# Kernel tuning notes

Hardware: AMD Instinct MI355X
Metric: run time of the kernel (lower is better)

Reference implementation:

```python
import jax, jax.numpy as jnp
import numpy as np

C = 128          # num_channel
NEI = 9          # patch_size / neighbor
R = NEI // 2     # displacement radius (4)
B, H, W = 4, 200, 200


def conv2d(x, w, b, pad):
    # x: [N,C,H,W], w: [O,I,kh,kw]
    y = jax.lax.conv_general_dilated(
        x, w, window_strides=(1, 1), padding=[(pad, pad), (pad, pad)],
        dimension_numbers=('NCHW', 'OIHW', 'NCHW'))
    return y + b[None, :, None, None]


def setup_inputs() -> dict:
    key = jax.random.key(0)
    ks = jax.random.split(key, 16)
    s = 0.02
    return {
        'feature_select': jax.random.normal(ks[0], (B, C, H, W), jnp.float32),
        'feature_current': jax.random.normal(ks[1], (B, C, H, W), jnp.float32),
        # embedding convs
        'ec1_w': jax.random.normal(ks[2], (64, C, 1, 1), jnp.float32) * s,
        'ec1_b': jnp.zeros((64,), jnp.float32),
        'ec2_w': jax.random.normal(ks[3], (64, 64, 3, 3), jnp.float32) * s,
        'ec2_b': jnp.zeros((64,), jnp.float32),
        # aggregation convs
        'ag1_w': jax.random.normal(ks[4], (64, C, 1, 1), jnp.float32) * s,
        'ag1_b': jnp.zeros((64,), jnp.float32),
        'ag2_w': jax.random.normal(ks[5], (32, 64, 3, 3), jnp.float32) * s,
        'ag2_b': jnp.zeros((32,), jnp.float32),
        'ag3_w': jax.random.normal(ks[6], (1, 32, 1, 1), jnp.float32) * s,
        'ag3_b': jnp.zeros((1,), jnp.float32),
    }


def reference(feature_select, feature_current, ec1_w, ec1_b, ec2_w, ec2_b,
              ag1_w, ag1_b, ag2_w, ag2_b, ag3_w, ag3_b):
    b, c, h, w = feature_select.shape
    # --- shared embedding network ---
    cat = jnp.concatenate([feature_select, feature_current], axis=0)
    e = jax.nn.relu(conv2d(cat, ec1_w, ec1_b, 0))
    e = jax.nn.relu(conv2d(e, ec2_w, ec2_b, 1))
    e_sel, e_cur = e[:b], e[b:]   # (torch code names these current/select, order follows concat)
    # --- correlation: 9x9 patch, kernel_size=1, zero-padded displaced neighbors ---
    ep = jnp.pad(e_cur, ((0, 0), (0, 0), (R, R), (R, R)))
    corr = []
    for di in range(-R, R + 1):
        for dj in range(-R, R + 1):
            nb = ep[:, :, R + di:R + di + h, R + dj:R + dj + w]
            corr.append(jnp.sum(e_sel * nb, axis=1))  # [b,h,w]
    weights = jax.nn.softmax(jnp.stack(corr, axis=1), axis=1)  # [b,81,h,w]
    # --- neighbor-weighted feature alignment ---
    sp = jnp.pad(feature_select, ((0, 0), (0, 0), (R, R), (R, R)))
    align = jnp.zeros_like(feature_select)
    k = 0
    for di in range(-R, R + 1):
        for dj in range(-R, R + 1):
            align = align + weights[:, k:k + 1] * sp[:, :, R + di:R + di + h, R + dj:R + dj + w]
            k += 1
    # --- aggregation: adaptive 2-way blend ---
    fc = jnp.concatenate([align, feature_current], axis=0)
    a = jax.nn.relu(conv2d(fc, ag1_w, ag1_b, 0))
    a = jax.nn.relu(conv2d(a, ag2_w, ag2_b, 1))
    a = jax.nn.relu(conv2d(a, ag3_w, ag3_b, 0))  # [2b,1,h,w]
    w2 = jax.nn.softmax(jnp.concatenate([a[:b], a[b:]], axis=1), axis=1)
    return w2[:, 0:1] * align + w2[:, 1:2] * feature_current
```

## Files before the change

### kernel.cpp

```cpp
#include <hip/hip_runtime.h>

namespace {
constexpr int H = 200, W = 200, HW = H * W;
constexpr int Bz = 4;
constexpr int PW = 208, PH = 202, PPLANE = PW * PH;
constexpr int EPW = 208, EPH = 208, EPL = EPW * EPH;
constexpr int WST = 88;
}

typedef __attribute__((ext_vector_type(8))) short bf16x8;
typedef __attribute__((ext_vector_type(4))) float f32x4;

__device__ inline ushort f2bf(float f) {
  unsigned u = __float_as_uint(f);
  u += 0x7fffu + ((u >> 16) & 1u);
  return (ushort)(u >> 16);
}

__global__ __launch_bounds__(256) void zero_k(uint4* __restrict__ p, int n) {
  int i = blockIdx.x * 256 + threadIdx.x;
  if (i < n) p[i] = uint4{0u, 0u, 0u, 0u};
}

__global__ __launch_bounds__(256) void wxform_k(const float* __restrict__ w,
                                                ushort* __restrict__ wb, int cout) {
  int i = blockIdx.x * 256 + threadIdx.x;
  int tot = cout * 64 * 9;
  if (i >= tot) return;
  int co = i / (64 * 9);
  int r = i % (64 * 9);
  int ci = r / 9, tap = r % 9;
  wb[(tap * cout + co) * 64 + ci] = f2bf(w[i]);
}

template <int CIN>
__global__ __launch_bounds__(256) void conv1x1_nhwc_k(
    const float* __restrict__ srcA, const float* __restrict__ srcB,
    const float* __restrict__ w, const float* __restrict__ bias,
    ushort* __restrict__ out) {
  __shared__ float wt[CIN * 64];
  for (int i = threadIdx.x; i < CIN * 64; i += 256) {
    int ci = i >> 6, co = i & 63;
    wt[i] = w[co * CIN + ci];
  }
  __syncthreads();
  int p = blockIdx.x * 256 + threadIdx.x;
  int bb = p / HW, pix = p % HW;
  const float* src =
      (bb < Bz ? srcA + (size_t)bb * CIN * HW : srcB + (size_t)(bb - Bz) * CIN * HW) + pix;
  float acc[64];
#pragma unroll
  for (int co = 0; co < 64; co++) acc[co] = bias[co];
  for (int ci = 0; ci < CIN; ci++) {
    float x = src[(size_t)ci * HW];
    const float4* w4 = (const float4*)&wt[ci * 64];
#pragma unroll
    for (int q = 0; q < 16; q++) {
      float4 wv = w4[q];
      acc[4 * q + 0] += x * wv.x;
      acc[4 * q + 1] += x * wv.y;
      acc[4 * q + 2] += x * wv.z;
      acc[4 * q + 3] += x * wv.w;
    }
  }
  int y = pix / W, x = pix % W;
  ushort* o = out + ((size_t)bb * PPLANE + (size_t)(y + 1) * PW + (x + 1)) * 64;
  uint4* o4 = (uint4*)o;
#pragma unroll
  for (int g = 0; g < 8; g++) {
    unsigned u0 = (unsigned)f2bf(fmaxf(acc[8 * g + 0], 0.f)) |
                  ((unsigned)f2bf(fmaxf(acc[8 * g + 1], 0.f)) << 16);
    unsigned u1 = (unsigned)f2bf(fmaxf(acc[8 * g + 2], 0.f)) |
                  ((unsigned)f2bf(fmaxf(acc[8 * g + 3], 0.f)) << 16);
    unsigned u2 = (unsigned)f2bf(fmaxf(acc[8 * g + 4], 0.f)) |
                  ((unsigned)f2bf(fmaxf(acc[8 * g + 5], 0.f)) << 16);
    unsigned u3 = (unsigned)f2bf(fmaxf(acc[8 * g + 6], 0.f)) |
                  ((unsigned)f2bf(fmaxf(acc[8 * g + 7], 0.f)) << 16);
    o4[g] = uint4{u0, u1, u2, u3};
  }
}

template <int COUT, bool NHWC>
__global__ __launch_bounds__(256) void conv3x3_mfma_k(
    const ushort* __restrict__ in, const ushort* __restrict__ wb,
    const float* __restrict__ bias, float* __restrict__ outf,
    ushort* __restrict__ outh) {
  constexpr int NF = COUT / 16;
  __shared__ ushort As[272 * 72];
  __shared__ ushort Bs[3 * COUT * 64];
  const int tile = blockIdx.x, img = blockIdx.y;
  const int pp0 = PW + tile * 256;
  const int tid = threadIdx.x, wave = tid >> 6, lane = tid & 63;
  const int lm = lane & 15, lq = lane >> 4;
  const ushort* inb = in + (size_t)img * PPLANE * 64;

  f32x4 acc[4][NF];
#pragma unroll
  for (int mf = 0; mf < 4; mf++)
#pragma unroll
    for (int nf = 0; nf < NF; nf++) acc[mf][nf] = f32x4{0.f, 0.f, 0.f, 0.f};

  for (int dy = 0; dy < 3; dy++) {
    __syncthreads();
    long abase = ((long)pp0 + (long)(dy - 1) * PW - 8) * 64;
    for (int i = tid; i < 272 * 8; i += 256) {
      int m = i >> 3, kseg = i & 7;
      uint4 v = *(const uint4*)(inb + abase + (long)m * 64 + kseg * 8);
      *(uint4*)&As[m * 72 + kseg * 8] = v;
    }
    for (int i = tid; i < 3 * COUT * 8; i += 256) {
      int dx = i / (COUT * 8);
      int r = i % (COUT * 8);
      int co = r >> 3, kseg = r & 7;
      uint4 v = *(const uint4*)(wb + (((size_t)(dy * 3 + dx) * COUT + co) << 6) + kseg * 8);
      *(uint4*)&Bs[(dx * COUT + co) * 64 + ((kseg ^ (co & 7)) * 8)] = v;
    }
    __syncthreads();
#pragma unroll
    for (int dx = 0; dx < 3; dx++) {
#pragma unroll
      for (int kc = 0; kc < 2; kc++) {
        bf16x8 bfr[NF];
#pragma unroll
        for (int nf = 0; nf < NF; nf++) {
          int n = nf * 16 + lm;
          int kb = kc * 4 + lq;
          bfr[nf] = *(const bf16x8*)&Bs[(dx * COUT + n) * 64 + ((kb ^ (n & 7)) * 8)];
        }
#pragma unroll
        for (int mf = 0; mf < 4; mf++) {
          int mo = (wave * 4 + mf) * 16 + lm;
          bf16x8 afr = *(const bf16x8*)&As[(mo + dx + 7) * 72 + kc * 32 + lq * 8];
#pragma unroll
          for (int nf = 0; nf < NF; nf++)
            acc[mf][nf] = __builtin_amdgcn_mfma_f32_16x16x32_bf16(afr, bfr[nf],
                                                                  acc[mf][nf], 0, 0, 0);
        }
      }
    }
  }
  float bv[NF];
#pragma unroll
  for (int nf = 0; nf < NF; nf++) bv[nf] = bias[nf * 16 + lm];
#pragma unroll
  for (int mf = 0; mf < 4; mf++) {
#pragma unroll
    for (int nf = 0; nf < NF; nf++) {
      int co = nf * 16 + lm;
#pragma unroll
      for (int r = 0; r < 4; r++) {
        int mo = pp0 + (wave * 4 + mf) * 16 + lq * 4 + r;
        int py = mo / PW, px = mo % PW;
        if (py >= 1 && py <= H && px >= 1 && px <= W) {
          float v = fmaxf(acc[mf][nf][r] + bv[nf], 0.f);
          if (NHWC) {
            ushort* eo = outh + (size_t)img * EPL * 64;
            eo[(((size_t)(py + 3)) * EPW + (px + 3)) * 64 + co] = f2bf(v);
          } else {
            outf[((size_t)img * COUT + co) * HW + (py - 1) * W + (px - 1)] = v;
          }
        }
      }
    }
  }
}

__global__ __launch_bounds__(128) void corr_mfma_k(
    const ushort* __restrict__ e, ushort* __restrict__ wgt) {
  __shared__ float S[2 * 16 * 91];
  const int wave = threadIdx.x >> 6, lane = threadIdx.x & 63;
  const int x0 = blockIdx.x * 16;
  const int y = blockIdx.y * 2 + wave;
  const int b = blockIdx.z;
  const int nl = lane & 15, kq = lane >> 4;
  const ushort* es = e + (size_t)b * EPL * 64;
  const ushort* ec = e + (size_t)(b + 4) * EPL * 64;
  size_t abase = ((size_t)(y + 4) * EPW + (size_t)(4 + x0 + nl)) * 64 + kq * 8;
  bf16x8 afr0 = *(const bf16x8*)(es + abase);
  bf16x8 afr1 = *(const bf16x8*)(es + abase + 32);
  float* Sw = &S[wave * 16 * 91];
  for (int di = 0; di < 9; di++) {
    const ushort* erow = ec + ((size_t)(y + di) * EPW + x0) * 64;
#pragma unroll
    for (int nh = 0; nh < 2; nh++) {
      f32x4 g = f32x4{0.f, 0.f, 0.f, 0.f};
      const ushort* bp = erow + (size_t)(nh * 16 + nl) * 64 + kq * 8;
      bf16x8 b0 = *(const bf16x8*)(bp);
      bf16x8 b1 = *(const bf16x8*)(bp + 32);
      g = __builtin_amdgcn_mfma_f32_16x16x32_bf16(afr0, b0, g, 0, 0, 0);
      g = __builtin_amdgcn_mfma_f32_16x16x32_bf16(afr1, b1, g, 0, 0, 0);
      int q = nh * 16 + nl;
#pragma unroll
      for (int r = 0; r < 4; r++) {
        int m = kq * 4 + r;
        int s = q - m;
        if (s >= 0 && s <= 8) Sw[m * 91 + di * 9 + s] = g[r];
      }
    }
  }
  int px = lane >> 2, lg = lane & 3;
  float* Sp = &Sw[px * 91];
  float mx = -1e30f;
  for (int k = lg; k < 81; k += 4) mx = fmaxf(mx, Sp[k]);
  mx = fmaxf(mx, __shfl_xor(mx, 1));
  mx = fmaxf(mx, __shfl_xor(mx, 2));
  float sum = 0.f;
  for (int k = lg; k < 81; k += 4) {
    float t = expf(Sp[k] - mx);
    Sp[k] = t;
    sum += t;
  }
  sum += __shfl_xor(sum, 1);
  sum += __shfl_xor(sum, 2);
  float rinv = 1.f / sum;
  if (x0 + px < W) {
    ushort* wp = wgt + ((size_t)b * 40000 + (size_t)y * W + x0 + px) * WST;
    for (int k = lg; k < 81; k += 4) wp[k] = f2bf(Sp[k] * rinv);
  }
}

__global__ __launch_bounds__(256) void align_mfma_k(
    const ushort* __restrict__ wgt, const float* __restrict__ fs,
    float* __restrict__ out) {
  __shared__ ushort F[32 * 392];
  __shared__ ushort WT[128 * WST];
  const int x0 = blockIdx.x * 16, y0 = blockIdx.y * 8;
  const int b = blockIdx.z & 3, cs = blockIdx.z >> 2;
  const int c0 = cs * 32;
  const int tid = threadIdx.x;
  {
    const ushort* wb = wgt + (size_t)b * 40000 * WST;
    for (int i = tid; i < 1408; i += 256) {
      int row = i / 176, rem = i % 176;
      size_t src = ((size_t)(y0 + row) * W + x0) * WST + (size_t)rem * 8;
      *(uint4*)&WT[(size_t)row * 16 * WST + rem * 8] = *(const uint4*)(wb + src);
    }
  }
  const float* fb = fs + ((size_t)b * 128 + c0) * HW;
  for (int i = tid; i < 32 * 392; i += 256) {
    int c = i / 392, rem = i % 392;
    int row = rem / 24, pos = rem % 24;
    int gy = y0 + row - 4, gx = x0 + pos - 4;
    float v = (rem < 384 && gy >= 0 && gy < H && gx >= 0 && gx < W)
                  ? fb[(size_t)c * HW + gy * W + gx] : 0.f;
    F[c * 392 + rem] = f2bf(v);
  }
  __syncthreads();
  const int wave = tid >> 6, lane = tid & 63;
  const int nl = lane & 15, kq = lane >> 4;
  f32x4 acc[2][2];
#pragma unroll
  for (int s = 0; s < 2; s++)
#pragma unroll
    for (int cg = 0; cg < 2; cg++) acc[s][cg] = f32x4{0.f, 0.f, 0.f, 0.f};

#pragma unroll
  for (int s = 0; s < 2; s++) {
    int r = wave * 2 + s;
    const ushort* wrow = &WT[(size_t)(r * 16 + nl) * WST];
    for (int di = 0; di < 9; di++) {
      union { bf16x8 v; ushort u[8]; } A;
#pragma unroll
      for (int j = 0; j < 8; j++) {
        int t = kq * 8 + j - nl;
        int tc = t < 0 ? 0 : (t > 8 ? 8 : t);
        ushort wv = wrow[di * 9 + tc];
        A.u[j] = (t == tc) ? wv : (ushort)0;
      }
#pragma unroll
      for (int cg = 0; cg < 2; cg++) {
        bf16x8 bfr = *(const bf16x8*)&F[(size_t)(cg * 16 + nl) * 392 +
                                        (r + di) * 24 + kq * 8];
        acc[s][cg] =
            __builtin_amdgcn_mfma_f32_16x16x32_bf16(A.v, bfr, acc[s][cg], 0, 0, 0);
      }
    }
  }
  int mg = lane >> 4;
  int x4 = x0 + mg * 4;
  if (x4 + 3 < W) {
#pragma unroll
    for (int s = 0; s < 2; s++) {
      int yy = y0 + wave * 2 + s;
#pragma unroll
      for (int cg = 0; cg < 2; cg++) {
        int cgl = c0 + cg * 16 + nl;
        float4 st = float4{acc[s][cg][0], acc[s][cg][1], acc[s][cg][2], acc[s][cg][3]};
        *(float4*)&out[((size_t)b * 128 + cgl) * HW + (size_t)yy * W + x4] = st;
      }
    }
  }
}

__global__ __launch_bounds__(256) void final_k(
    const float* __restrict__ a2, const float* __restrict__ w3,
    const float* __restrict__ b3, const float* __restrict__ alignb,
    const float* __restrict__ fcur, float* __restrict__ out) {
  int p = blockIdx.x * 256 + threadIdx.x;
  int bb = p / HW, pix = p % HW;
  const float* aS = a2 + (size_t)bb * 32 * HW + pix;
  const float* aC = a2 + (size_t)(bb + Bz) * 32 * HW + pix;
  float s0 = b3[0], s1 = b3[0];
#pragma unroll
  for (int c = 0; c < 32; c++) {
    float wv = w3[c];
    s0 += wv * aS[(size_t)c * HW];
    s1 += wv * aC[(size_t)c * HW];
  }
  s0 = fmaxf(s0, 0.f);
  s1 = fmaxf(s1, 0.f);
  float m = fmaxf(s0, s1);
  float e0 = expf(s0 - m), e1 = expf(s1 - m);
  float inv = 1.f / (e0 + e1);
  float p0 = e0 * inv, p1 = e1 * inv;
  const float* al = alignb + (size_t)bb * 128 * HW + pix;
  const float* fc = fcur + (size_t)bb * 128 * HW + pix;
  float* o = out + (size_t)bb * 128 * HW + pix;
#pragma unroll 4
  for (int c = 0; c < 128; c++)
    o[(size_t)c * HW] = p0 * al[(size_t)c * HW] + p1 * fc[(size_t)c * HW];
}

extern "C" void kernel_launch(void* const* d_in, const int* in_sizes, int n_in,
                              void* d_out, int out_size, void* d_ws, size_t ws_size,
                              hipStream_t stream) {
  const float* fsel = (const float*)d_in[0];
  const float* fcur = (const float*)d_in[1];
  const float* ec1_w = (const float*)d_in[2];
  const float* ec1_b = (const float*)d_in[3];
  const float* ec2_w = (const float*)d_in[4];
  const float* ec2_b = (const float*)d_in[5];
  const float* ag1_w = (const float*)d_in[6];
  const float* ag1_b = (const float*)d_in[7];
  const float* ag2_w = (const float*)d_in[8];
  const float* ag2_b = (const float*)d_in[9];
  const float* ag3_w = (const float*)d_in[10];
  const float* ag3_b = (const float*)d_in[11];

  char* ws = (char*)d_ws;
  size_t off = 4096;
  ushort* padbuf = (ushort*)(ws + off);
  size_t padbuf_bytes = (size_t)8 * PPLANE * 64 * 2;
  off += padbuf_bytes;
  ushort* epad = (ushort*)(ws + off);
  size_t epad_bytes = (size_t)8 * EPL * 64 * 2;
  off += epad_bytes + 4096;
  ushort* wgtb = (ushort*)(ws + off);
  off += (size_t)4 * 40000 * WST * 2 + 4096;
  float* alignb = (float*)(ws + off);
  off += (size_t)4 * 128 * HW * 4;
  ushort* wb1 = (ushort*)(ws + off);
  off += 9 * 64 * 64 * 2;
  ushort* wb2 = (ushort*)(ws + off);
  off += 9 * 32 * 64 * 2;
  float* a2 = (float*)epad;
  float* outp = (float*)d_out;

  dim3 blk(256);
  const int MTILES = (200 * PW + 255) / 256;

  wxform_k<<<(9 * 64 * 64 + 255) / 256, blk, 0, stream>>>(ec2_w, wb1, 64);
  wxform_k<<<(9 * 32 * 64 + 255) / 256, blk, 0, stream>>>(ag2_w, wb2, 32);
  {
    int nz = (int)((padbuf_bytes + epad_bytes) / 16);
    zero_k<<<(nz + 255) / 256, blk, 0, stream>>>((uint4*)padbuf, nz);
  }
  conv1x1_nhwc_k<128><<<1250, blk, 0, stream>>>(fsel, fcur, ec1_w, ec1_b, padbuf);
  conv3x3_mfma_k<64, true><<<dim3(MTILES, 8), blk, 0, stream>>>(
      padbuf, wb1, ec2_b, nullptr, epad);
  corr_mfma_k<<<dim3(13, 100, 4), dim3(128), 0, stream>>>(epad, wgtb);
  align_mfma_k<<<dim3(13, 25, 16), blk, 0, stream>>>(wgtb, fsel, alignb);
  conv1x1_nhwc_k<128><<<1250, blk, 0, stream>>>(alignb, fcur, ag1_w, ag1_b, padbuf);
  conv3x3_mfma_k<32, false><<<dim3(MTILES, 8), blk, 0, stream>>>(
      padbuf, wb2, ag2_b, a2, nullptr);
  final_k<<<625, blk, 0, stream>>>(a2, ag3_w, ag3_b, alignb, fcur, outp);
}
```

Before: 902.0 us.

## Replace MFMA align kernel with VALU kernel using planar softmax weights

The correlation kernel now writes the softmax weights in a planar layout (81 planes per batch) instead of a per-pixel strided layout. The alignment kernel drops the banded-matrix MFMA formulation, which wasted most MMA lanes on zero padding. It becomes a VALU kernel where each block covers a 16x8 tile for all 128 channels in four chunks of 32, loading the weights once and keeping feature_select in fp32 in LDS. Blocks are also remapped across the XCDs for locality. This cuts redundant weight loads and the bf16 rounding of the features, at the cost of more scalar FMA work and larger LDS usage.

New measurement: 1.082 ms. 1.2x slower.

```diff
diff --git a/kernel.cpp b/kernel.cpp
--- a/kernel.cpp
+++ b/kernel.cpp
@@ -5,7 +5,6 @@
 constexpr int Bz = 4;
 constexpr int PW = 208, PH = 202, PPLANE = PW * PH;
 constexpr int EPW = 208, EPH = 208, EPL = EPW * EPH;
-constexpr int WST = 88;
 }
 
 typedef __attribute__((ext_vector_type(8))) short bf16x8;
@@ -214,79 +213,92 @@
   sum += __shfl_xor(sum, 2);
   float rinv = 1.f / sum;
   if (x0 + px < W) {
-    ushort* wp = wgt + ((size_t)b * 40000 + (size_t)y * W + x0 + px) * WST;
-    for (int k = lg; k < 81; k += 4) wp[k] = f2bf(Sp[k] * rinv);
-  }
-}
-
-__global__ __launch_bounds__(256) void align_mfma_k(
+    ushort* wp = wgt + (size_t)b * 81 * HW + (size_t)y * W + x0 + px;
+    for (int k = lg; k < 81; k += 4) wp[(size_t)k * HW] = f2bf(Sp[k] * rinv);
+  }
+}
+
+__global__ __launch_bounds__(256, 2) void align_valu_k(
     const ushort* __restrict__ wgt, const float* __restrict__ fs,
     float* __restrict__ out) {
-  __shared__ ushort F[32 * 392];
-  __shared__ ushort WT[128 * WST];
-  const int x0 = blockIdx.x * 16, y0 = blockIdx.y * 8;
-  const int b = blockIdx.z & 3, cs = blockIdx.z >> 2;
-  const int c0 = cs * 32;
+  __shared__ ushort Ws[81 * 128];
+  __shared__ float Fs[32 * 448];
   const int tid = threadIdx.x;
+  int orig = blockIdx.x + 25 * (blockIdx.y + 13 * blockIdx.z);
+  int xcd = orig & 7, idx = orig >> 3;
+  int wgid = (xcd < 4 ? xcd * 163 : 652 + (xcd - 4) * 162) + idx;
+  int by = wgid % 25;
+  int t2 = wgid / 25;
+  int bx = t2 % 13;
+  int b = t2 / 13;
+  const int x0 = bx * 16, y0 = by * 8;
+
   {
-    const ushort* wb = wgt + (size_t)b * 40000 * WST;
-    for (int i = tid; i < 1408; i += 256) {
-      int row = i / 176, rem = i % 176;
-      size_t src = ((size_t)(y0 + row) * W + x0) * WST + (size_t)rem * 8;
-      *(uint4*)&WT[(size_t)row * 16 * WST + rem * 8] = *(const uint4*)(wb + src);
-    }
-  }
-  const float* fb = fs + ((size_t)b * 128 + c0) * HW;
-  for (int i = tid; i < 32 * 392; i += 256) {
-    int c = i / 392, rem = i % 392;
-    int row = rem / 24, pos = rem % 24;
-    int gy = y0 + row - 4, gx = x0 + pos - 4;
-    float v = (rem < 384 && gy >= 0 && gy < H && gx >= 0 && gx < W)
-                  ? fb[(size_t)c * HW + gy * W + gx] : 0.f;
-    F[c * 392 + rem] = f2bf(v);
-  }
-  __syncthreads();
-  const int wave = tid >> 6, lane = tid & 63;
-  const int nl = lane & 15, kq = lane >> 4;
-  f32x4 acc[2][2];
-#pragma unroll
-  for (int s = 0; s < 2; s++)
-#pragma unroll
-    for (int cg = 0; cg < 2; cg++) acc[s][cg] = f32x4{0.f, 0.f, 0.f, 0.f};
-
-#pragma unroll
-  for (int s = 0; s < 2; s++) {
-    int r = wave * 2 + s;
-    const ushort* wrow = &WT[(size_t)(r * 16 + nl) * WST];
-    for (int di = 0; di < 9; di++) {
-      union { bf16x8 v; ushort u[8]; } A;
-#pragma unroll
-      for (int j = 0; j < 8; j++) {
-        int t = kq * 8 + j - nl;
-        int tc = t < 0 ? 0 : (t > 8 ? 8 : t);
-        ushort wv = wrow[di * 9 + tc];
-        A.u[j] = (t == tc) ? wv : (ushort)0;
-      }
-#pragma unroll
-      for (int cg = 0; cg < 2; cg++) {
-        bf16x8 bfr = *(const bf16x8*)&F[(size_t)(cg * 16 + nl) * 392 +
-                                        (r + di) * 24 + kq * 8];
-        acc[s][cg] =
-            __builtin_amdgcn_mfma_f32_16x16x32_bf16(A.v, bfr, acc[s][cg], 0, 0, 0);
-      }
-    }
-  }
-  int mg = lane >> 4;
-  int x4 = x0 + mg * 4;
-  if (x4 + 3 < W) {
-#pragma unroll
-    for (int s = 0; s < 2; s++) {
-      int yy = y0 + wave * 2 + s;
-#pragma unroll
-      for (int cg = 0; cg < 2; cg++) {
-        int cgl = c0 + cg * 16 + nl;
-        float4 st = float4{acc[s][cg][0], acc[s][cg][1], acc[s][cg][2], acc[s][cg][3]};
-        *(float4*)&out[((size_t)b * 128 + cgl) * HW + (size_t)yy * W + x4] = st;
+    const ushort* wb = wgt + (size_t)b * 81 * HW;
+    for (int i = tid; i < 81 * 128; i += 256) {
+      int k = i >> 7, px = i & 127;
+      int gy = y0 + (px >> 4);
+      int gx = x0 + (px & 15);
+      if (gx > W - 1) gx = W - 1;
+      Ws[i] = wb[(size_t)k * HW + gy * W + gx];
+    }
+  }
+  const int xq = tid & 3, yy = (tid >> 2) & 7, cl = tid >> 5;
+  const int pxw = yy * 16 + xq * 4;
+  const int xb = x0 + xq * 4;
+  for (int r = 0; r < 4; ++r) {
+    if (r) __syncthreads();
+    {
+      const float* fb = fs + ((size_t)b * 128 + r * 32) * HW;
+      for (int i = tid; i < 32 * 384; i += 256) {
+        int cc = i / 384, rem = i % 384;
+        int row = rem / 24, col = rem % 24;
+        int gy = y0 - 4 + row, gx = x0 - 4 + col;
+        float v = 0.f;
+        if (gy >= 0 && gy < H && gx >= 0 && gx < W)
+          v = fb[(size_t)cc * HW + gy * W + gx];
+        Fs[cc * 448 + row * 28 + col] = v;
+      }
+    }
+    __syncthreads();
+    float acc[4][4];
+#pragma unroll
+    for (int j = 0; j < 4; j++)
+#pragma unroll
+      for (int p = 0; p < 4; p++) acc[j][p] = 0.f;
+    for (int di = 0; di < 9; ++di) {
+      float fr[4][12];
+#pragma unroll
+      for (int j = 0; j < 4; ++j) {
+        const float4* fp =
+            (const float4*)&Fs[(cl * 4 + j) * 448 + (yy + di) * 28 + xq * 4];
+        float4 f0 = fp[0], f1 = fp[1], f2 = fp[2];
+        fr[j][0] = f0.x; fr[j][1] = f0.y; fr[j][2] = f0.z; fr[j][3] = f0.w;
+        fr[j][4] = f1.x; fr[j][5] = f1.y; fr[j][6] = f1.z; fr[j][7] = f1.w;
+        fr[j][8] = f2.x; fr[j][9] = f2.y; fr[j][10] = f2.z; fr[j][11] = f2.w;
+      }
+#pragma unroll
+      for (int dj = 0; dj < 9; ++dj) {
+        uint2 wv = *(const uint2*)&Ws[(di * 9 + dj) * 128 + pxw];
+        float w0 = __uint_as_float(wv.x << 16);
+        float w1 = __uint_as_float(wv.x & 0xffff0000u);
+        float w2 = __uint_as_float(wv.y << 16);
+        float w3 = __uint_as_float(wv.y & 0xffff0000u);
+#pragma unroll
+        for (int j = 0; j < 4; ++j) {
+          acc[j][0] += w0 * fr[j][dj + 0];
+          acc[j][1] += w1 * fr[j][dj + 1];
+          acc[j][2] += w2 * fr[j][dj + 2];
+          acc[j][3] += w3 * fr[j][dj + 3];
+        }
+      }
+    }
+    if (xb < W) {
+#pragma unroll
+      for (int j = 0; j < 4; ++j) {
+        int c = r * 32 + cl * 4 + j;
+        *(float4*)&out[((size_t)b * 128 + c) * HW + (size_t)(y0 + yy) * W + xb] =
+            float4{acc[j][0], acc[j][1], acc[j][2], acc[j][3]};
       }
     }
   }
@@ -346,7 +358,7 @@
   size_t epad_bytes = (size_t)8 * EPL * 64 * 2;
   off += epad_bytes + 4096;
   ushort* wgtb = (ushort*)(ws + off);
-  off += (size_t)4 * 40000 * WST * 2 + 4096;
+  off += (size_t)4 * 81 * HW * 2 + 4096;
   float* alignb = (float*)(ws + off);
   off += (size_t)4 * 128 * HW * 4;
   ushort* wb1 = (ushort*)(ws + off);
@@ -369,7 +381,7 @@
   conv3x3_mfma_k<64, true><<<dim3(MTILES, 8), blk, 0, stream>>>(
       padbuf, wb1, ec2_b, nullptr, epad);
   corr_mfma_k<<<dim3(13, 100, 4), dim3(128), 0, stream>>>(epad, wgtb);
-  align_mfma_k<<<dim3(13, 25, 16), blk, 0, stream>>>(wgtb, fsel, alignb);
+  align_valu_k<<<dim3(25, 13, 4), blk, 0, stream>>>(wgtb, fsel, alignb);
   conv1x1_nhwc_k<128><<<1250, blk, 0, stream>>>(alignb, fcur, ag1_w, ag1_b, padbuf);
   conv3x3_mfma_k<32, false><<<dim3(MTILES, 8), blk, 0, stream>>>(
       padbuf, wb2, ag2_b, a2, nullptr);
```

## Store softmax weights planar and rebuild align kernel with banded-weight LDS staging

Applied to the files above, without the earlier changes.

The correlation kernel now writes softmax weights in a planar [b][81][HW] layout instead of a per-pixel strided layout. The align kernel is rewritten to use 16x16 pixel tiles over 16 channels per block. It builds a banded weight matrix in LDS for each row displacement and prefetches the next displacement's weights into registers. The grid is a flat 1D launch ordered so that the batch/half index varies fastest, and occupancy is hinted at 3 blocks. This drops the per-lane select/clamp construction of A fragments and shrinks the weight buffer, at the cost of two barriers per displacement, strided per-plane weight reads, and more redundant feature halo loads for smaller channel groups.

Result: faster. 874.5 us (-3.1%).

```diff
diff --git a/kernel.cpp b/kernel.cpp
--- a/kernel.cpp
+++ b/kernel.cpp
@@ -5,7 +5,6 @@
 constexpr int Bz = 4;
 constexpr int PW = 208, PH = 202, PPLANE = PW * PH;
 constexpr int EPW = 208, EPH = 208, EPL = EPW * EPH;
-constexpr int WST = 88;
 }
 
 typedef __attribute__((ext_vector_type(8))) short bf16x8;
@@ -214,79 +213,92 @@
   sum += __shfl_xor(sum, 2);
   float rinv = 1.f / sum;
   if (x0 + px < W) {
-    ushort* wp = wgt + ((size_t)b * 40000 + (size_t)y * W + x0 + px) * WST;
-    for (int k = lg; k < 81; k += 4) wp[k] = f2bf(Sp[k] * rinv);
-  }
-}
-
-__global__ __launch_bounds__(256) void align_mfma_k(
+    ushort* wp = wgt + (size_t)b * 81 * HW + (size_t)y * W + x0 + px;
+    for (int k = lg; k < 81; k += 4) wp[(size_t)k * HW] = f2bf(Sp[k] * rinv);
+  }
+}
+
+__global__ __launch_bounds__(256, 3) void align_mfma2_k(
     const ushort* __restrict__ wgt, const float* __restrict__ fs,
     float* __restrict__ out) {
-  __shared__ ushort F[32 * 392];
-  __shared__ ushort WT[128 * WST];
-  const int x0 = blockIdx.x * 16, y0 = blockIdx.y * 8;
-  const int b = blockIdx.z & 3, cs = blockIdx.z >> 2;
-  const int c0 = cs * 32;
+  __shared__ alignas(16) ushort As2[16 * 16 * 40];
+  __shared__ alignas(16) ushort Fs2[24 * 16 * 40];
   const int tid = threadIdx.x;
+  int bid = blockIdx.x;
+  int p = bid & 7;
+  int rank = bid >> 3;
+  const int b = p >> 1, h = p & 1;
+  const int cgi = rank & 3;
+  int tile = rank >> 2;
+  const int ty = tile / 13, tx = tile % 13;
+  const int x0 = tx * 16, y0 = ty * 16;
+  const int c0 = (h * 4 + cgi) * 16;
+
+  for (int i = tid; i < 1280; i += 256) *(uint4*)&As2[i * 8] = uint4{0u, 0u, 0u, 0u};
+
+  const int srow = tid >> 4, sm = tid & 15;
+  const bool sval = (y0 + srow < H) && (x0 + sm < W);
+  const ushort* wrow =
+      wgt + (size_t)b * 81 * HW + (size_t)(y0 + srow) * W + (x0 + sm);
+  ushort wv[9];
+  if (sval) {
+#pragma unroll
+    for (int dj = 0; dj < 9; dj++) wv[dj] = wrow[(size_t)dj * HW];
+  }
+
   {
-    const ushort* wb = wgt + (size_t)b * 40000 * WST;
-    for (int i = tid; i < 1408; i += 256) {
-      int row = i / 176, rem = i % 176;
-      size_t src = ((size_t)(y0 + row) * W + x0) * WST + (size_t)rem * 8;
-      *(uint4*)&WT[(size_t)row * 16 * WST + rem * 8] = *(const uint4*)(wb + src);
-    }
-  }
-  const float* fb = fs + ((size_t)b * 128 + c0) * HW;
-  for (int i = tid; i < 32 * 392; i += 256) {
-    int c = i / 392, rem = i % 392;
-    int row = rem / 24, pos = rem % 24;
-    int gy = y0 + row - 4, gx = x0 + pos - 4;
-    float v = (rem < 384 && gy >= 0 && gy < H && gx >= 0 && gx < W)
-                  ? fb[(size_t)c * HW + gy * W + gx] : 0.f;
-    F[c * 392 + rem] = f2bf(v);
+    const float* fb = fs + ((size_t)b * 128 + c0) * HW;
+    for (int i = tid; i < 24 * 16 * 32; i += 256) {
+      int k = i & 31;
+      int c = (i >> 5) & 15;
+      int rf = i >> 9;
+      int gy = y0 - 4 + rf, gx = x0 - 4 + k;
+      float v = 0.f;
+      if (k < 24 && gy >= 0 && gy < H && gx >= 0 && gx < W)
+        v = fb[(size_t)c * HW + (size_t)gy * W + gx];
+      Fs2[(rf * 16 + c) * 40 + k] = f2bf(v);
+    }
   }
   __syncthreads();
-  const int wave = tid >> 6, lane = tid & 63;
+
+  const int lane = tid & 63, wave = tid >> 6;
   const int nl = lane & 15, kq = lane >> 4;
-  f32x4 acc[2][2];
-#pragma unroll
-  for (int s = 0; s < 2; s++)
-#pragma unroll
-    for (int cg = 0; cg < 2; cg++) acc[s][cg] = f32x4{0.f, 0.f, 0.f, 0.f};
-
-#pragma unroll
-  for (int s = 0; s < 2; s++) {
-    int r = wave * 2 + s;
-    const ushort* wrow = &WT[(size_t)(r * 16 + nl) * WST];
-    for (int di = 0; di < 9; di++) {
-      union { bf16x8 v; ushort u[8]; } A;
-#pragma unroll
-      for (int j = 0; j < 8; j++) {
-        int t = kq * 8 + j - nl;
-        int tc = t < 0 ? 0 : (t > 8 ? 8 : t);
-        ushort wv = wrow[di * 9 + tc];
-        A.u[j] = (t == tc) ? wv : (ushort)0;
-      }
-#pragma unroll
-      for (int cg = 0; cg < 2; cg++) {
-        bf16x8 bfr = *(const bf16x8*)&F[(size_t)(cg * 16 + nl) * 392 +
-                                        (r + di) * 24 + kq * 8];
-        acc[s][cg] =
-            __builtin_amdgcn_mfma_f32_16x16x32_bf16(A.v, bfr, acc[s][cg], 0, 0, 0);
-      }
-    }
-  }
-  int mg = lane >> 4;
-  int x4 = x0 + mg * 4;
-  if (x4 + 3 < W) {
-#pragma unroll
-    for (int s = 0; s < 2; s++) {
-      int yy = y0 + wave * 2 + s;
-#pragma unroll
-      for (int cg = 0; cg < 2; cg++) {
-        int cgl = c0 + cg * 16 + nl;
-        float4 st = float4{acc[s][cg][0], acc[s][cg][1], acc[s][cg][2], acc[s][cg][3]};
-        *(float4*)&out[((size_t)b * 128 + cgl) * HW + (size_t)yy * W + x4] = st;
+  f32x4 acc[4];
+#pragma unroll
+  for (int rr = 0; rr < 4; rr++) acc[rr] = f32x4{0.f, 0.f, 0.f, 0.f};
+
+  for (int di = 0; di < 9; ++di) {
+    if (sval) {
+#pragma unroll
+      for (int dj = 0; dj < 9; dj++)
+        As2[(srow * 16 + sm) * 40 + sm + dj] = wv[dj];
+    }
+    if (di < 8 && sval) {
+      const ushort* wn = wrow + (size_t)((di + 1) * 9) * HW;
+#pragma unroll
+      for (int dj = 0; dj < 9; dj++) wv[dj] = wn[(size_t)dj * HW];
+    }
+    __syncthreads();
+#pragma unroll
+    for (int rr = 0; rr < 4; ++rr) {
+      int row = wave * 4 + rr;
+      bf16x8 af = *(const bf16x8*)&As2[(row * 16 + nl) * 40 + kq * 8];
+      int rf = row + di;
+      bf16x8 bf = *(const bf16x8*)&Fs2[(rf * 16 + nl) * 40 + kq * 8];
+      acc[rr] = __builtin_amdgcn_mfma_f32_16x16x32_bf16(af, bf, acc[rr], 0, 0, 0);
+    }
+    __syncthreads();
+  }
+
+  const int xs = x0 + kq * 4;
+  if (xs + 3 < W) {
+    int c = c0 + nl;
+#pragma unroll
+    for (int rr = 0; rr < 4; ++rr) {
+      int y = y0 + wave * 4 + rr;
+      if (y < H) {
+        *(float4*)&out[((size_t)b * 128 + c) * HW + (size_t)y * W + xs] =
+            float4{acc[rr][0], acc[rr][1], acc[rr][2], acc[rr][3]};
       }
     }
   }
@@ -346,7 +358,7 @@
   size_t epad_bytes = (size_t)8 * EPL * 64 * 2;
   off += epad_bytes + 4096;
   ushort* wgtb = (ushort*)(ws + off);
-  off += (size_t)4 * 40000 * WST * 2 + 4096;
+  off += (size_t)4 * 81 * HW * 2 + 4096;
   float* alignb = (float*)(ws + off);
   off += (size_t)4 * 128 * HW * 4;
   ushort* wb1 = (ushort*)(ws + off);
@@ -369,7 +381,7 @@
   conv3x3_mfma_k<64, true><<<dim3(MTILES, 8), blk, 0, stream>>>(
       padbuf, wb1, ec2_b, nullptr, epad);
   corr_mfma_k<<<dim3(13, 100, 4), dim3(128), 0, stream>>>(epad, wgtb);
-  align_mfma_k<<<dim3(13, 25, 16), blk, 0, stream>>>(wgtb, fsel, alignb);
+  align_mfma2_k<<<5408, blk, 0, stream>>>(wgtb, fsel, alignb);
   conv1x1_nhwc_k<128><<<1250, blk, 0, stream>>>(alignb, fcur, ag1_w, ag1_b, padbuf);
   conv3x3_mfma_k<32, false><<<dim3(MTILES, 8), blk, 0, stream>>>(
       padbuf, wb2, ag2_b, a2, nullptr);
```
